# Kernel optimization log

Hardware: AMD Instinct MI355X
Metric: run time of the kernel (lower is better)

## Reference

```python
import jax, jax.numpy as jnp
import numpy as np

N = 1048576   # total tokens
B = 4096      # number of segments (batch)
D = 256       # in_features
H = 128       # mlp hidden
TEMP = 1.0


def setup_inputs() -> dict:
    key = jax.random.key(0)
    k1, k2, k3, k4 = jax.random.split(key, 4)
    x = jax.random.normal(k1, (N, D), dtype=jnp.float32)
    segment_ids = jnp.sort(jax.random.randint(k2, (N,), 0, B))
    W1 = jax.random.normal(k3, (D, H), dtype=jnp.float32) * (1.0 / np.sqrt(D))
    b1 = jnp.zeros((H,), dtype=jnp.float32)
    W2 = jax.random.normal(k4, (H, 1), dtype=jnp.float32) * (1.0 / np.sqrt(H))
    b2 = jnp.zeros((1,), dtype=jnp.float32)
    return {"x": x, "segment_ids": segment_ids, "W1": W1, "b1": b1, "W2": W2, "b2": b2}


def reference(x, segment_ids, W1, b1, W2, b2):
    # MLP attention logits: [N, 1]
    logits = jnp.tanh(x @ W1 + b1) @ W2 + b2          # [N, 1]
    s = logits[:, 0] / TEMP                           # [N]
    # numerically stable per-segment softmax via segment max/sum
    seg_max = jax.ops.segment_max(s, segment_ids, num_segments=B)   # [B]
    z = jnp.exp(s - seg_max[segment_ids])                            # [N]
    denom = jax.ops.segment_sum(z, segment_ids, num_segments=B)     # [B]
    attention_weights = (z / denom[segment_ids])[:, None]            # [N, 1]
    # segment weighted-sum pooling -> context vectors [B, D]
    context_vectors = jax.ops.segment_sum(attention_weights * x, segment_ids, num_segments=B)
    return context_vectors, attention_weights
```

## Files before the change

### kernel.cpp

```cpp
#include <hip/hip_runtime.h>
#include <hip/hip_bf16.h>
#include <math.h>

#define N_TOK 1048576
#define BSEG  4096
#define DIM   256
#define HID   128

typedef __attribute__((ext_vector_type(8))) short short8;
typedef __attribute__((ext_vector_type(4))) short short4v;
typedef __attribute__((ext_vector_type(4))) float f32x4;

__device__ __forceinline__ short f2bf(float f) {
    union { float f; unsigned u; } v; v.f = f;
    unsigned r = v.u + 0x7fff + ((v.u >> 16) & 1);
    return (short)(r >> 16);
}
__device__ __forceinline__ float bf2f(short s) {
    union { unsigned u; float f; } v;
    v.u = ((unsigned)(unsigned short)s) << 16;
    return v.f;
}

__global__ void prep_w1t(const float* __restrict__ W1, short* __restrict__ W1T) {
    int i = blockIdx.x * blockDim.x + threadIdx.x;
    int h = i >> 8;
    int k = i & 255;
    W1T[i] = f2bf(W1[k * HID + h]);
}

__launch_bounds__(256, 3)
__global__ void main_kernel(const float* __restrict__ x,
                            const int*  __restrict__ seg,
                            const short* __restrict__ W1T,
                            const float* __restrict__ b1,
                            const float* __restrict__ W2,
                            const float* __restrict__ b2,
                            float* __restrict__ ctx,
                            float* __restrict__ zout,
                            float* __restrict__ denom) {
    __shared__ __align__(16) short x_lds[64 * 264];
    __shared__ float s_part[4][64];
    __shared__ float z_lds[64];
    __shared__ int   seg_lds[64];

    const int tid  = threadIdx.x;
    const int wv   = tid >> 6;
    const int lane = tid & 63;
    const int q    = lane >> 4;
    const int c    = lane & 15;
    const long base_tok = (long)blockIdx.x * 64;

    if (tid < 64) seg_lds[tid] = seg[base_tok + tid];

    const float4* xg = reinterpret_cast<const float4*>(x) + base_tok * 64;
#pragma unroll
    for (int it = 0; it < 16; ++it) {
        int flat  = it * 256 + tid;
        int token = flat >> 6, kq = flat & 63;
        float4 v = xg[flat];
        short4v p = { f2bf(v.x), f2bf(v.y), f2bf(v.z), f2bf(v.w) };
        *reinterpret_cast<short4v*>(&x_lds[token * 264 + kq * 4]) = p;
    }

    short8 bf[2][8];
#pragma unroll
    for (int ti = 0; ti < 2; ++ti) {
        int t = wv + 4 * ti;
#pragma unroll
        for (int kk = 0; kk < 8; ++kk) {
            bf[ti][kk] = *reinterpret_cast<const short8*>(
                W1T + (t * 16 + c) * 256 + kk * 32 + q * 8);
        }
    }
    const float b1v0 = b1[wv * 16 + c];
    const float b1v1 = b1[(wv + 4) * 16 + c];
    const float w2v0 = W2[wv * 16 + c];
    const float w2v1 = W2[(wv + 4) * 16 + c];
    const float b2s  = b2[0];

    __syncthreads();

#pragma unroll
    for (int tt = 0; tt < 4; ++tt) {
        f32x4 acc0 = {0.f, 0.f, 0.f, 0.f};
        f32x4 acc1 = {0.f, 0.f, 0.f, 0.f};
        const short* arow = &x_lds[(tt * 16 + c) * 264 + q * 8];
#pragma unroll
        for (int kk = 0; kk < 8; ++kk) {
            short8 a = *reinterpret_cast<const short8*>(arow + kk * 32);
            acc0 = __builtin_amdgcn_mfma_f32_16x16x32_bf16(a, bf[0][kk], acc0, 0, 0, 0);
            acc1 = __builtin_amdgcn_mfma_f32_16x16x32_bf16(a, bf[1][kk], acc1, 0, 0, 0);
        }
        float part[4];
#pragma unroll
        for (int r = 0; r < 4; ++r) {
            float h0 = tanhf(acc0[r] + b1v0);
            float h1 = tanhf(acc1[r] + b1v1);
            part[r] = h0 * w2v0 + h1 * w2v1;
        }
#pragma unroll
        for (int r = 0; r < 4; ++r) {
            float v = part[r];
            v += __shfl_xor(v, 1);
            v += __shfl_xor(v, 2);
            v += __shfl_xor(v, 4);
            v += __shfl_xor(v, 8);
            part[r] = v;
        }
        if (c == 0) {
            float4 st = make_float4(part[0], part[1], part[2], part[3]);
            *reinterpret_cast<float4*>(&s_part[wv][tt * 16 + q * 4]) = st;
        }
    }
    __syncthreads();

    if (tid < 64) {
        float s = s_part[0][tid] + s_part[1][tid] + s_part[2][tid] + s_part[3][tid] + b2s;
        float z = __expf(s) * 0.f + expf(s);
        z_lds[tid] = z;
        zout[base_tok + tid] = z;
    }
    __syncthreads();

    {
        const int j = tid;
        float acc = 0.f;
        int prev = seg_lds[0];
#pragma unroll 4
        for (int n = 0; n < 64; ++n) {
            int sg = seg_lds[n];
            if (sg != prev) {
                atomicAdd(&ctx[(long)prev * DIM + j], acc);
                acc = 0.f;
                prev = sg;
            }
            acc += z_lds[n] * bf2f(x_lds[n * 264 + j]);
        }
        atomicAdd(&ctx[(long)prev * DIM + j], acc);
    }
    if (tid == 0) {
        float az = 0.f;
        int pv = seg_lds[0];
        for (int n = 0; n < 64; ++n) {
            int sg = seg_lds[n];
            if (sg != pv) { atomicAdd(&denom[pv], az); az = 0.f; pv = sg; }
            az += z_lds[n];
        }
        atomicAdd(&denom[pv], az);
    }
}

__global__ void finalize(float* __restrict__ out, const float* __restrict__ denom,
                         const int* __restrict__ seg) {
    long idx = (long)blockIdx.x * 256 + threadIdx.x;
    const long BD = (long)BSEG * DIM;
    if (idx < BD) {
        float dn = denom[idx >> 8];
        float v = out[idx];
        out[idx] = dn > 0.f ? v / dn : 0.f;
    } else {
        long n = idx - BD;
        float dn = denom[seg[n]];
        float z = out[idx];
        out[idx] = dn > 0.f ? z / dn : 0.f;
    }
}

extern "C" void kernel_launch(void* const* d_in, const int* in_sizes, int n_in,
                              void* d_out, int out_size, void* d_ws, size_t ws_size,
                              hipStream_t stream) {
    const float* x  = (const float*)d_in[0];
    const int*   sg = (const int*)d_in[1];
    const float* W1 = (const float*)d_in[2];
    const float* b1 = (const float*)d_in[3];
    const float* W2 = (const float*)d_in[4];
    const float* b2 = (const float*)d_in[5];
    float* out = (float*)d_out;

    short* W1T   = (short*)d_ws;
    float* denom = (float*)((char*)d_ws + 65536);
    const long BD = (long)BSEG * DIM;

    hipMemsetAsync(out, 0, BD * sizeof(float), stream);
    hipMemsetAsync(denom, 0, BSEG * sizeof(float), stream);

    prep_w1t<<<(HID * DIM) / 256, 256, 0, stream>>>(W1, W1T);
    main_kernel<<<N_TOK / 64, 256, 0, stream>>>(x, sg, W1T, b1, W2, b2,
                                                out, out + BD, denom);
    finalize<<<(int)((BD + N_TOK) / 256), 256, 0, stream>>>(out, denom, sg);
}
```

Baseline: 1.445 ms.

## Stream x through double-buffered async LDS loads in persistent 32-token chunks

Each block now handles 64 chunks of 32 tokens instead of one 64-token tile. The next chunk of fp32 x is copied into a second LDS buffer with global_load_lds while the current chunk runs its MFMA and pooling, using an XOR swizzle to avoid bank conflicts. Conversion to bf16 moves to LDS read time, and pooling and denominator partial sums carry across chunks, so far fewer global atomics are issued. tanhf is replaced by an exp-based fast tanh. The costs are 64 KB of fp32 LDS per block, a drop from 3 to 2 blocks per CU, and a loss of parallelism from running only 512 blocks.

```diff
diff --git a/kernel.cpp b/kernel.cpp
--- a/kernel.cpp
+++ b/kernel.cpp
@@ -1,14 +1,17 @@
 #include <hip/hip_runtime.h>
 #include <hip/hip_bf16.h>
 #include <math.h>
+#include <stdint.h>
 
 #define N_TOK 1048576
 #define BSEG  4096
 #define DIM   256
 #define HID   128
+#define TPC   32
+#define CPB   64
+#define GRID  (N_TOK / (TPC * CPB))
 
 typedef __attribute__((ext_vector_type(8))) short short8;
-typedef __attribute__((ext_vector_type(4))) short short4v;
 typedef __attribute__((ext_vector_type(4))) float f32x4;
 
 __device__ __forceinline__ short f2bf(float f) {
@@ -16,11 +19,22 @@
     unsigned r = v.u + 0x7fff + ((v.u >> 16) & 1);
     return (short)(r >> 16);
 }
-__device__ __forceinline__ float bf2f(short s) {
-    union { unsigned u; float f; } v;
-    v.u = ((unsigned)(unsigned short)s) << 16;
-    return v.f;
-}
+
+__device__ __forceinline__ float fast_tanh(float v) {
+    float e = __expf(2.f * v);
+    return 1.f - __fdividef(2.f, e + 1.f);
+}
+
+typedef __attribute__((address_space(1))) const unsigned int as1_u32;
+typedef __attribute__((address_space(3))) unsigned int as3_u32;
+__device__ __forceinline__ void gload16(const void* g, void* l) {
+    __builtin_amdgcn_global_load_lds((as1_u32*)g, (as3_u32*)l, 16, 0, 0);
+}
+
+#define BAR_LGKM() do { asm volatile("s_waitcnt lgkmcnt(0)" ::: "memory"); \
+    __builtin_amdgcn_s_barrier(); asm volatile("" ::: "memory"); } while (0)
+#define BAR_ALL() do { asm volatile("s_waitcnt vmcnt(0) lgkmcnt(0)" ::: "memory"); \
+    __builtin_amdgcn_s_barrier(); asm volatile("" ::: "memory"); } while (0)
 
 __global__ void prep_w1t(const float* __restrict__ W1, short* __restrict__ W1T) {
     int i = blockIdx.x * blockDim.x + threadIdx.x;
@@ -29,7 +43,7 @@
     W1T[i] = f2bf(W1[k * HID + h]);
 }
 
-__launch_bounds__(256, 3)
+__launch_bounds__(256, 2)
 __global__ void main_kernel(const float* __restrict__ x,
                             const int*  __restrict__ seg,
                             const short* __restrict__ W1T,
@@ -39,28 +53,35 @@
                             float* __restrict__ ctx,
                             float* __restrict__ zout,
                             float* __restrict__ denom) {
-    __shared__ __align__(16) short x_lds[64 * 264];
-    __shared__ float s_part[4][64];
-    __shared__ float z_lds[64];
-    __shared__ int   seg_lds[64];
+    __shared__ __align__(16) float x_lds[2][TPC * DIM];
+    __shared__ __align__(16) int   seg_all[TPC * CPB];
+    __shared__ float s_part[4][TPC];
+    __shared__ float z_lds[TPC];
 
     const int tid  = threadIdx.x;
     const int wv   = tid >> 6;
     const int lane = tid & 63;
     const int q    = lane >> 4;
     const int c    = lane & 15;
-    const long base_tok = (long)blockIdx.x * 64;
-
-    if (tid < 64) seg_lds[tid] = seg[base_tok + tid];
-
-    const float4* xg = reinterpret_cast<const float4*>(x) + base_tok * 64;
-#pragma unroll
-    for (int it = 0; it < 16; ++it) {
-        int flat  = it * 256 + tid;
-        int token = flat >> 6, kq = flat & 63;
-        float4 v = xg[flat];
-        short4v p = { f2bf(v.x), f2bf(v.y), f2bf(v.z), f2bf(v.w) };
-        *reinterpret_cast<short4v*>(&x_lds[token * 264 + kq * 4]) = p;
+    const long tok0 = (long)blockIdx.x * (TPC * CPB);
+
+    char* xb0 = (char*)&x_lds[0][0];
+    char* xb1 = (char*)&x_lds[1][0];
+    const int drb = wv * 1024 + lane * 16;
+
+    {
+        const char* g = (const char*)(x + tok0 * DIM);
+#pragma unroll
+        for (int i = 0; i < 8; ++i) {
+            int dr = drb + i * 4096;
+            int sr = dr ^ (((dr >> 10) & 7) << 4);
+            gload16(g + sr, xb0 + i * 4096 + wv * 1024);
+        }
+        const char* sg = (const char*)(seg + tok0);
+        char* sb = (char*)seg_all;
+#pragma unroll
+        for (int i = 0; i < 2; ++i)
+            gload16(sg + i * 4096 + drb, sb + i * 4096 + wv * 1024);
     }
 
     short8 bf[2][8];
@@ -68,10 +89,9 @@
     for (int ti = 0; ti < 2; ++ti) {
         int t = wv + 4 * ti;
 #pragma unroll
-        for (int kk = 0; kk < 8; ++kk) {
+        for (int kk = 0; kk < 8; ++kk)
             bf[ti][kk] = *reinterpret_cast<const short8*>(
                 W1T + (t * 16 + c) * 256 + kk * 32 + q * 8);
-        }
     }
     const float b1v0 = b1[wv * 16 + c];
     const float b1v1 = b1[(wv + 4) * 16 + c];
@@ -79,76 +99,100 @@
     const float w2v1 = W2[(wv + 4) * 16 + c];
     const float b2s  = b2[0];
 
-    __syncthreads();
-
-#pragma unroll
-    for (int tt = 0; tt < 4; ++tt) {
-        f32x4 acc0 = {0.f, 0.f, 0.f, 0.f};
-        f32x4 acc1 = {0.f, 0.f, 0.f, 0.f};
-        const short* arow = &x_lds[(tt * 16 + c) * 264 + q * 8];
-#pragma unroll
-        for (int kk = 0; kk < 8; ++kk) {
-            short8 a = *reinterpret_cast<const short8*>(arow + kk * 32);
-            acc0 = __builtin_amdgcn_mfma_f32_16x16x32_bf16(a, bf[0][kk], acc0, 0, 0, 0);
-            acc1 = __builtin_amdgcn_mfma_f32_16x16x32_bf16(a, bf[1][kk], acc1, 0, 0, 0);
-        }
-        float part[4];
-#pragma unroll
-        for (int r = 0; r < 4; ++r) {
-            float h0 = tanhf(acc0[r] + b1v0);
-            float h1 = tanhf(acc1[r] + b1v1);
-            part[r] = h0 * w2v0 + h1 * w2v1;
-        }
-#pragma unroll
-        for (int r = 0; r < 4; ++r) {
-            float v = part[r];
-            v += __shfl_xor(v, 1);
-            v += __shfl_xor(v, 2);
-            v += __shfl_xor(v, 4);
-            v += __shfl_xor(v, 8);
-            part[r] = v;
-        }
-        if (c == 0) {
-            float4 st = make_float4(part[0], part[1], part[2], part[3]);
-            *reinterpret_cast<float4*>(&s_part[wv][tt * 16 + q * 4]) = st;
-        }
-    }
-    __syncthreads();
-
-    if (tid < 64) {
-        float s = s_part[0][tid] + s_part[1][tid] + s_part[2][tid] + s_part[3][tid] + b2s;
-        float z = __expf(s) * 0.f + expf(s);
-        z_lds[tid] = z;
-        zout[base_tok + tid] = z;
-    }
-    __syncthreads();
-
-    {
-        const int j = tid;
-        float acc = 0.f;
-        int prev = seg_lds[0];
-#pragma unroll 4
-        for (int n = 0; n < 64; ++n) {
-            int sg = seg_lds[n];
-            if (sg != prev) {
-                atomicAdd(&ctx[(long)prev * DIM + j], acc);
-                acc = 0.f;
-                prev = sg;
-            }
-            acc += z_lds[n] * bf2f(x_lds[n * 264 + j]);
-        }
-        atomicAdd(&ctx[(long)prev * DIM + j], acc);
-    }
-    if (tid == 0) {
-        float az = 0.f;
-        int pv = seg_lds[0];
-        for (int n = 0; n < 64; ++n) {
-            int sg = seg_lds[n];
-            if (sg != pv) { atomicAdd(&denom[pv], az); az = 0.f; pv = sg; }
-            az += z_lds[n];
-        }
-        atomicAdd(&denom[pv], az);
-    }
+    float pool_acc = 0.f;
+    int   prev  = seg[tok0];
+    float az    = 0.f;
+    int   prevd = prev;
+
+    BAR_ALL();
+
+    for (int ci = 0; ci < CPB; ++ci) {
+        char* cur = (ci & 1) ? xb1 : xb0;
+        if (ci + 1 < CPB) {
+            const char* g = (const char*)(x + (tok0 + (long)(ci + 1) * TPC) * DIM);
+            char* nb = (ci & 1) ? xb0 : xb1;
+#pragma unroll
+            for (int i = 0; i < 8; ++i) {
+                int dr = drb + i * 4096;
+                int sr = dr ^ (((dr >> 10) & 7) << 4);
+                gload16(g + sr, nb + i * 4096 + wv * 1024);
+            }
+        }
+
+#pragma unroll
+        for (int tt = 0; tt < 2; ++tt) {
+            f32x4 acc0 = {0.f, 0.f, 0.f, 0.f};
+            f32x4 acc1 = {0.f, 0.f, 0.f, 0.f};
+            const int row = tt * 16 + c;
+            const char* p0 = cur + row * 1024 + ((q * 32) ^ ((c & 7) << 4));
+            const char* p1 = (const char*)((uintptr_t)p0 ^ 16u);
+#pragma unroll
+            for (int kk = 0; kk < 8; ++kk) {
+                f32x4 v0 = *(const f32x4*)(p0 + kk * 128);
+                f32x4 v1 = *(const f32x4*)(p1 + kk * 128);
+                short8 a = { f2bf(v0[0]), f2bf(v0[1]), f2bf(v0[2]), f2bf(v0[3]),
+                             f2bf(v1[0]), f2bf(v1[1]), f2bf(v1[2]), f2bf(v1[3]) };
+                acc0 = __builtin_amdgcn_mfma_f32_16x16x32_bf16(a, bf[0][kk], acc0, 0, 0, 0);
+                acc1 = __builtin_amdgcn_mfma_f32_16x16x32_bf16(a, bf[1][kk], acc1, 0, 0, 0);
+            }
+            float part[4];
+#pragma unroll
+            for (int r = 0; r < 4; ++r) {
+                float h0 = fast_tanh(acc0[r] + b1v0);
+                float h1 = fast_tanh(acc1[r] + b1v1);
+                part[r] = h0 * w2v0 + h1 * w2v1;
+            }
+#pragma unroll
+            for (int r = 0; r < 4; ++r) {
+                float v = part[r];
+                v += __shfl_xor(v, 1);
+                v += __shfl_xor(v, 2);
+                v += __shfl_xor(v, 4);
+                v += __shfl_xor(v, 8);
+                part[r] = v;
+            }
+            if (c == 0)
+                *reinterpret_cast<float4*>(&s_part[wv][tt * 16 + q * 4]) =
+                    make_float4(part[0], part[1], part[2], part[3]);
+        }
+        BAR_LGKM();
+
+        if (tid < TPC) {
+            float s = s_part[0][tid] + s_part[1][tid] + s_part[2][tid]
+                    + s_part[3][tid] + b2s;
+            float z = __expf(s);
+            z_lds[tid] = z;
+            zout[tok0 + (long)ci * TPC + tid] = z;
+        }
+        BAR_LGKM();
+
+        {
+            const int* sgl = &seg_all[ci * TPC];
+            const int j4 = tid * 4;
+#pragma unroll 8
+            for (int n = 0; n < TPC; ++n) {
+                int s = sgl[n];
+                float xv = *(const float*)(cur + n * 1024 + (j4 ^ ((n & 7) << 4)));
+                if (s != prev) {
+                    atomicAdd(&ctx[(long)prev * DIM + tid], pool_acc);
+                    pool_acc = 0.f;
+                    prev = s;
+                }
+                pool_acc += z_lds[n] * xv;
+            }
+        }
+        if (tid == 0) {
+            const int* sgl = &seg_all[ci * TPC];
+            for (int n = 0; n < TPC; ++n) {
+                int s = sgl[n];
+                if (s != prevd) { atomicAdd(&denom[prevd], az); az = 0.f; prevd = s; }
+                az += z_lds[n];
+            }
+        }
+        BAR_ALL();
+    }
+    atomicAdd(&ctx[(long)prev * DIM + tid], pool_acc);
+    if (tid == 0) atomicAdd(&denom[prevd], az);
 }
 
 __global__ void finalize(float* __restrict__ out, const float* __restrict__ denom,
@@ -186,7 +230,7 @@
     hipMemsetAsync(denom, 0, BSEG * sizeof(float), stream);
 
     prep_w1t<<<(HID * DIM) / 256, 256, 0, stream>>>(W1, W1T);
-    main_kernel<<<N_TOK / 64, 256, 0, stream>>>(x, sg, W1T, b1, W2, b2,
-                                                out, out + BD, denom);
+    main_kernel<<<GRID, 256, 0, stream>>>(x, sg, W1T, b1, W2, b2,
+                                          out, out + BD, denom);
     finalize<<<(int)((BD + N_TOK) / 256), 256, 0, stream>>>(out, denom, sg);
 }
```

After: 1.620 ms. +12.2%, slower.
